# Kernel tuning notes

Measured on AMD Instinct MI355X. Metric: run time of the kernel, lower is better.

Reference implementation:

```python
import jax, jax.numpy as jnp
import numpy as np

B, S, H, NH, MLP = 4, 2048, 768, 12, 3072
HD = H // NH  # 64
EPS = 1e-6


def layernorm(x, w, b):
    m = jnp.mean(x, axis=-1, keepdims=True)
    v = jnp.mean(jnp.square(x - m), axis=-1, keepdims=True)
    return (x - m) * jax.lax.rsqrt(v + EPS) * w + b


def setup_inputs() -> dict:
    key = jax.random.key(0)
    ks = jax.random.split(key, 16)
    s = 0.02
    return {
        "x": jax.random.normal(ks[0], (B, S, H), dtype=jnp.float32),
        "ln1_w": jnp.ones((H,), jnp.float32),
        "ln1_b": jnp.zeros((H,), jnp.float32),
        "wq": jax.random.normal(ks[1], (H, H), jnp.float32) * s,
        "bq": jnp.zeros((H,), jnp.float32),
        "wk": jax.random.normal(ks[2], (H, H), jnp.float32) * s,
        "bk": jnp.zeros((H,), jnp.float32),
        "wv": jax.random.normal(ks[3], (H, H), jnp.float32) * s,
        "bv": jnp.zeros((H,), jnp.float32),
        "wo": jax.random.normal(ks[4], (H, H), jnp.float32) * s,
        "bo": jnp.zeros((H,), jnp.float32),
        "ln2_w": jnp.ones((H,), jnp.float32),
        "ln2_b": jnp.zeros((H,), jnp.float32),
        "w1": jax.random.normal(ks[5], (H, MLP), jnp.float32) * s,
        "b1": jnp.zeros((MLP,), jnp.float32),
        "w2": jax.random.normal(ks[6], (MLP, H), jnp.float32) * s,
        "b2": jnp.zeros((H,), jnp.float32),
    }


def reference(x, ln1_w, ln1_b, wq, bq, wk, bk, wv, bv, wo, bo,
              ln2_w, ln2_b, w1, b1, w2, b2):
    # --- attention sub-block (pre-norm) ---
    h = x
    xn = layernorm(x, ln1_w, ln1_b)
    q = (xn @ wq + bq).reshape(B, S, NH, HD)
    k = (xn @ wk + bk).reshape(B, S, NH, HD)
    v = (xn @ wv + bv).reshape(B, S, NH, HD)
    scores = jnp.einsum('bqhd,bkhd->bhqk', q, k) / jnp.sqrt(jnp.float32(HD))
    probs = jax.nn.softmax(scores, axis=-1)  # [B,NH,S,S] materialized, as in source
    ctx = jnp.einsum('bhqk,bkhd->bqhd', probs, v).reshape(B, S, H)
    x = ctx @ wo + bo + h
    # --- MLP sub-block (pre-norm) ---
    h = x
    xn = layernorm(x, ln2_w, ln2_b)
    y = jax.nn.gelu(xn @ w1 + b1, approximate=False)  # nn.GELU default = exact erf
    x = y @ w2 + b2 + h
    return x
```

## Files before the change

kernel.cpp:

```cpp
#include <hip/hip_runtime.h>
#include <hip/hip_bf16.h>

#define B_ 4
#define S_ 2048
#define H_ 768
#define NH_ 12
#define HD_ 64
#define MLP_ 3072
#define M_ (B_*S_)

typedef float f32x4 __attribute__((ext_vector_type(4)));
typedef short bf16x8 __attribute__((ext_vector_type(8)));

__device__ __forceinline__ short f2bf(float f) {
  union { float f; unsigned u; } x; x.f = f;
  unsigned r = (x.u + 0x7fffu + ((x.u >> 16) & 1u)) >> 16;
  return (short)(unsigned short)r;
}

__device__ __forceinline__ float exp2g(float x) {
  float r; asm("v_exp_f32 %0, %1" : "=v"(r) : "v"(x)); return r;
}
__device__ __forceinline__ float rcpg(float x) {
  float r; asm("v_rcp_f32 %0, %1" : "=v"(r) : "v"(x)); return r;
}
__device__ __forceinline__ unsigned cvtpk(float a, float b) {
  unsigned r; asm("v_cvt_pk_bf16_f32 %0, %1, %2" : "=v"(r) : "v"(a), "v"(b)); return r;
}

typedef __attribute__((address_space(1))) const void gvoid;
typedef __attribute__((address_space(3))) void lvoid;
__device__ __forceinline__ void async16(const void* g, void* l) {
  __builtin_amdgcn_global_load_lds((gvoid*)g, (lvoid*)l, 16, 0, 0);
}

__device__ __forceinline__ int xcd_swz(int h, int nwg) {
  const int q = nwg >> 3, r = nwg & 7;
  const int xc = h & 7, i = h >> 3;
  return (xc < r ? xc * (q + 1) : r * (q + 1) + (xc - r) * q) + i;
}

__global__ __launch_bounds__(256)
void tcast(const float* __restrict__ in, short* __restrict__ out, int K, int N) {
  __shared__ float tile[32][33];
  const int n0 = blockIdx.x * 32, k0 = blockIdx.y * 32;
  const int tx = threadIdx.x, ty = threadIdx.y;
#pragma unroll
  for (int i = 0; i < 4; ++i)
    tile[ty * 4 + i][tx] = in[(size_t)(k0 + ty * 4 + i) * N + n0 + tx];
  __syncthreads();
#pragma unroll
  for (int i = 0; i < 4; ++i)
    out[(size_t)(n0 + ty * 4 + i) * K + k0 + tx] = f2bf(tile[tx][ty * 4 + i]);
}

__global__ __launch_bounds__(256)
void tcast4(const float* __restrict__ i0, const float* __restrict__ i1,
            const float* __restrict__ i2, const float* __restrict__ i3,
            short* __restrict__ o0, short* __restrict__ o1,
            short* __restrict__ o2, short* __restrict__ o3) {
  __shared__ float tile[32][33];
  const int z = blockIdx.z;
  const float* in = (z == 0) ? i0 : (z == 1) ? i1 : (z == 2) ? i2 : i3;
  short* out = (z == 0) ? o0 : (z == 1) ? o1 : (z == 2) ? o2 : o3;
  const int n0 = blockIdx.x * 32, k0 = blockIdx.y * 32;
  const int tx = threadIdx.x, ty = threadIdx.y;
#pragma unroll
  for (int i = 0; i < 4; ++i)
    tile[ty * 4 + i][tx] = in[(size_t)(k0 + ty * 4 + i) * 768 + n0 + tx];
  __syncthreads();
#pragma unroll
  for (int i = 0; i < 4; ++i)
    out[(size_t)(n0 + ty * 4 + i) * 768 + k0 + tx] = f2bf(tile[tx][ty * 4 + i]);
}

__device__ __forceinline__ float block_sum256(float v) {
  __shared__ float red[4];
#pragma unroll
  for (int o = 32; o > 0; o >>= 1) v += __shfl_down(v, o);
  if ((threadIdx.x & 63) == 0) red[threadIdx.x >> 6] = v;
  __syncthreads();
  v = red[0] + red[1] + red[2] + red[3];
  __syncthreads();
  return v;
}

__global__ __launch_bounds__(256)
void ln_fwd(const float* __restrict__ xin, const float* __restrict__ g,
            const float* __restrict__ bt, short* __restrict__ o) {
  const int row = blockIdx.x, t = threadIdx.x;
  const float* xr = xin + (size_t)row * H_;
  const float v0 = xr[t], v1 = xr[t + 256], v2 = xr[t + 512];
  const float mean = block_sum256(v0 + v1 + v2) * (1.0f / H_);
  const float d0 = v0 - mean, d1 = v1 - mean, d2 = v2 - mean;
  const float var = block_sum256(d0 * d0 + d1 * d1 + d2 * d2) * (1.0f / H_);
  const float rstd = rsqrtf(var + 1e-6f);
  short* orow = o + (size_t)row * H_;
  orow[t]       = f2bf(d0 * rstd * g[t] + bt[t]);
  orow[t + 256] = f2bf(d1 * rstd * g[t + 256] + bt[t + 256]);
  orow[t + 512] = f2bf(d2 * rstd * g[t + 512] + bt[t + 512]);
}

#define QSCALE 0.18033688011112042f
template<int MODE>
__global__ __launch_bounds__(256)
void gemm_bt(const short* __restrict__ A, const short* __restrict__ Bw,
             int K, int N,
             const float* __restrict__ b0, const float* __restrict__ b1,
             const float* __restrict__ b2,
             const float* __restrict__ resid,
             float* __restrict__ outf, short* __restrict__ outh,
             short* __restrict__ oq, short* __restrict__ ok2, short* __restrict__ ov) {
  __shared__ short As[2][128 * 64];
  __shared__ short Bs[2][64 * 64];
  const int tid = threadIdx.x;
  const int wv = tid >> 6, lane = tid & 63;
  const int lo = lane & 15, hi = lane >> 4;
  const int wr = wv >> 1, wc = wv & 1;

  const int GX = gridDim.x;
  const int logical = xcd_swz(blockIdx.y * GX + blockIdx.x, GX * gridDim.y);
  const int bn = logical % GX, bm = logical / GX;

  const short* Ab = A + (size_t)bm * 128 * K;
  const short* Bb = Bw + (size_t)bn * 64 * K;
  const int srow = lane >> 3;
  const int scol = ((lane & 7) ^ srow) * 8;

  auto stage = [&](int buf, int kt) {
#pragma unroll
    for (int c = 0; c < 4; ++c) {
      const int rb = wv * 32 + c * 8;
      async16(Ab + (size_t)(rb + srow) * K + kt + scol, &As[buf][rb * 64]);
    }
#pragma unroll
    for (int c = 0; c < 2; ++c) {
      const int rb = wv * 16 + c * 8;
      async16(Bb + (size_t)(rb + srow) * K + kt + scol, &Bs[buf][rb * 64]);
    }
  };

  f32x4 acc[4][2] = {};
  stage(0, 0);
  const int nIt = K >> 6;
  for (int it = 0; it < nIt; ++it) {
    __syncthreads();
    if (it + 1 < nIt) stage((it + 1) & 1, (it + 1) << 6);
    const short* as = As[it & 1];
    const short* bs = Bs[it & 1];
#pragma unroll
    for (int ks = 0; ks < 2; ++ks) {
      const int rc = (((ks * 4 + hi) ^ (lo & 7)) * 8);
      bf16x8 af[4], bfr[2];
#pragma unroll
      for (int m = 0; m < 4; ++m)
        af[m] = *(const bf16x8*)&as[(wr * 64 + m * 16 + lo) * 64 + rc];
#pragma unroll
      for (int n = 0; n < 2; ++n)
        bfr[n] = *(const bf16x8*)&bs[(wc * 32 + n * 16 + lo) * 64 + rc];
#pragma unroll
      for (int m = 0; m < 4; ++m)
#pragma unroll
        for (int n = 0; n < 2; ++n)
          acc[m][n] = __builtin_amdgcn_mfma_f32_16x16x32_bf16(af[m], bfr[n], acc[m][n], 0, 0, 0);
    }
  }
  const int colBase = bn * 64 + wc * 32;
  const int rowBase = bm * 128 + wr * 64;
#pragma unroll
  for (int m = 0; m < 4; ++m) {
#pragma unroll
    for (int n = 0; n < 2; ++n) {
#pragma unroll
      for (int r = 0; r < 4; ++r) {
        const int row = rowBase + m * 16 + hi * 4 + r;
        const int col = colBase + n * 16 + lo;
        float val = acc[m][n][r];
        if (MODE == 0) {
          const int which = col / H_;
          const int nn = col - which * H_;
          val += (which == 0 ? b0 : which == 1 ? b1 : b2)[nn];
          if (which == 0) val *= QSCALE;
          const int h = nn >> 6, d = nn & 63;
          const int bI = row >> 11, s = row & (S_ - 1);
          const short bv16 = f2bf(val);
          if (which == 2) {
            const int sl = s & 63;
            const int pc = ((sl >> 4) & 1) * 32 + ((sl >> 2) & 3) * 8
                         + ((sl >> 5) & 1) * 4 + (sl & 3);
            ov[(((size_t)bI * NH_ + h) * HD_ + d) * S_ + (s & ~63) + pc] = bv16;
          } else {
            short* dst = (which == 0 ? oq : ok2);
            dst[(((size_t)bI * NH_ + h) * S_ + s) * HD_ + d] = bv16;
          }
        } else if (MODE == 1) {
          val += b0[col] + resid[(size_t)row * N + col];
          outf[(size_t)row * N + col] = val;
        } else {
          val += b0[col];
          const float u = val * (0.7978845608f + 0.0356774081f * val * val);
          const float e = exp2g(-2.885390082f * u);
          val = val * rcpg(1.0f + e);
          outh[(size_t)row * N + col] = f2bf(val);
        }
      }
    }
  }
}

__global__ __launch_bounds__(256)
void attn_fwd(const short* __restrict__ qbuf, const short* __restrict__ kbuf,
              const short* __restrict__ vbuf, short* __restrict__ ctx) {
  __shared__ short Ks[2][8 * 512];
  __shared__ short Vt[2][8 * 512];
  const int tid = threadIdx.x;
  const int wv = tid >> 6, lane = tid & 63;
  const int lo = lane & 15, hi = lane >> 4;
  const int logical = xcd_swz(blockIdx.y * 32 + blockIdx.x, 32 * 48);
  const int qt = logical & 31, bh = logical >> 5;
  const int bI = bh / NH_, h = bh - bI * NH_;
  const size_t baseBH = (size_t)bh * S_ * HD_;
  const int q0 = qt * 64 + wv * 16;

  bf16x8 qf[2];
#pragma unroll
  for (int ks = 0; ks < 2; ++ks)
    qf[ks] = *(const bf16x8*)&qbuf[baseBH + (size_t)(q0 + lo) * HD_ + ks * 32 + hi * 8];

  f32x4 accc[4] = {};
  f32x4 accS = {};
  float mrow = 0.0f;

  const short oo = (lo == 0) ? (short)0x3F80 : (short)0;
  const bf16x8 onesf = {oo, oo, oo, oo, oo, oo, oo, oo};

  const short* ksrc = kbuf + baseBH + (size_t)(wv * 16 + lo) * HD_ + hi * 8;
  const short* vsrc = vbuf + baseBH + (size_t)(wv * 16 + lo) * S_ + hi * 8;
  const int dst0 = wv * 1024 + lane * 8;

  bf16x8 kreg0, kreg1, vreg0, vreg1;
  kreg0 = *(const bf16x8*)(ksrc);
  kreg1 = *(const bf16x8*)(ksrc + 32);
  vreg0 = *(const bf16x8*)(vsrc);
  vreg1 = *(const bf16x8*)(vsrc + 32);
  *(bf16x8*)&Ks[0][dst0] = kreg0;
  *(bf16x8*)&Ks[0][dst0 + 512] = kreg1;
  *(bf16x8*)&Vt[0][dst0] = vreg0;
  *(bf16x8*)&Vt[0][dst0 + 512] = vreg1;
  kreg0 = *(const bf16x8*)(ksrc + (size_t)64 * HD_);
  kreg1 = *(const bf16x8*)(ksrc + (size_t)64 * HD_ + 32);
  vreg0 = *(const bf16x8*)(vsrc + 64);
  vreg1 = *(const bf16x8*)(vsrc + 64 + 32);
  __syncthreads();

  for (int t = 0; t < S_ / 64; ++t) {
    const int cur = t & 1, nxt = cur ^ 1;
    const short* ks = Ks[cur];
    const short* vt = Vt[cur];
    f32x4 sc[4];
    __builtin_amdgcn_s_setprio(1);
#pragma unroll
    for (int nk = 0; nk < 4; ++nk) {
      f32x4 z = {0.f, 0.f, 0.f, 0.f};
#pragma unroll
      for (int k2 = 0; k2 < 2; ++k2) {
        bf16x8 kf = *(const bf16x8*)&ks[(nk * 2 + k2) * 512 + lane * 8];
        z = __builtin_amdgcn_mfma_f32_16x16x32_bf16(kf, qf[k2], z, 0, 0, 0);
      }
      sc[nk] = z;
    }
    __builtin_amdgcn_s_setprio(0);
    *(bf16x8*)&Ks[nxt][dst0] = kreg0;
    *(bf16x8*)&Ks[nxt][dst0 + 512] = kreg1;
    *(bf16x8*)&Vt[nxt][dst0] = vreg0;
    *(bf16x8*)&Vt[nxt][dst0 + 512] = vreg1;
    {
      const int tn = (t + 2 < S_ / 64) ? t + 2 : S_ / 64 - 1;
      const short* kp = ksrc + (size_t)tn * 64 * HD_;
      kreg0 = *(const bf16x8*)(kp);
      kreg1 = *(const bf16x8*)(kp + 32);
      const short* vp = vsrc + tn * 64;
      vreg0 = *(const bf16x8*)(vp);
      vreg1 = *(const bf16x8*)(vp + 32);
    }
    const float m0 = fmaxf(fmaxf(sc[0][0], sc[0][1]), fmaxf(sc[0][2], sc[0][3]));
    const float m1 = fmaxf(fmaxf(sc[1][0], sc[1][1]), fmaxf(sc[1][2], sc[1][3]));
    const float m2 = fmaxf(fmaxf(sc[2][0], sc[2][1]), fmaxf(sc[2][2], sc[2][3]));
    const float m3 = fmaxf(fmaxf(sc[3][0], sc[3][1]), fmaxf(sc[3][2], sc[3][3]));
    float mx = fmaxf(fmaxf(m0, m1), fmaxf(m2, m3));
#pragma unroll
    for (int nk = 0; nk < 4; ++nk)
#pragma unroll
      for (int r = 0; r < 4; ++r)
        sc[nk][r] = exp2g(sc[nk][r] - mrow);
    if (!__all(mx <= mrow + 8.0f)) {
      mx = fmaxf(mx, __shfl_xor(mx, 16));
      mx = fmaxf(mx, __shfl_xor(mx, 32));
      const float mnew = fmaxf(mrow, mx);
      const float alpha = exp2g(mrow - mnew);
#pragma unroll
      for (int nk = 0; nk < 4; ++nk)
#pragma unroll
        for (int r = 0; r < 4; ++r) sc[nk][r] *= alpha;
#pragma unroll
      for (int r = 0; r < 4; ++r) {
        const float aA = __shfl(alpha, hi * 4 + r);
        accS[r] *= aA;
#pragma unroll
        for (int nd = 0; nd < 4; ++nd) accc[nd][r] *= aA;
      }
      mrow = mnew;
    }
    union PU { unsigned u[4]; bf16x8 v; } pa0, pa1;
    pa0.u[0] = cvtpk(sc[0][0], sc[0][1]); pa0.u[1] = cvtpk(sc[0][2], sc[0][3]);
    pa0.u[2] = cvtpk(sc[2][0], sc[2][1]); pa0.u[3] = cvtpk(sc[2][2], sc[2][3]);
    pa1.u[0] = cvtpk(sc[1][0], sc[1][1]); pa1.u[1] = cvtpk(sc[1][2], sc[1][3]);
    pa1.u[2] = cvtpk(sc[3][0], sc[3][1]); pa1.u[3] = cvtpk(sc[3][2], sc[3][3]);
    __builtin_amdgcn_s_setprio(1);
    accS = __builtin_amdgcn_mfma_f32_16x16x32_bf16(pa0.v, onesf, accS, 0, 0, 0);
    accS = __builtin_amdgcn_mfma_f32_16x16x32_bf16(pa1.v, onesf, accS, 0, 0, 0);
#pragma unroll
    for (int nd = 0; nd < 4; ++nd) {
      bf16x8 vf0 = *(const bf16x8*)&vt[(nd * 2 + 0) * 512 + lane * 8];
      accc[nd] = __builtin_amdgcn_mfma_f32_16x16x32_bf16(pa0.v, vf0, accc[nd], 0, 0, 0);
      bf16x8 vf1 = *(const bf16x8*)&vt[(nd * 2 + 1) * 512 + lane * 8];
      accc[nd] = __builtin_amdgcn_mfma_f32_16x16x32_bf16(pa1.v, vf1, accc[nd], 0, 0, 0);
    }
    __builtin_amdgcn_s_setprio(0);
    __syncthreads();
  }
#pragma unroll
  for (int r = 0; r < 4; ++r) {
    const float inv = 1.0f / __shfl(accS[r], hi << 4);
    const int srow = q0 + hi * 4 + r;
    const size_t rowoff = ((size_t)bI * S_ + srow) * H_ + h * HD_;
#pragma unroll
    for (int nd = 0; nd < 4; ++nd)
      ctx[rowoff + nd * 16 + lo] = f2bf(accc[nd][r] * inv);
  }
}

extern "C" void kernel_launch(void* const* d_in, const int* in_sizes, int n_in,
                              void* d_out, int out_size, void* d_ws, size_t ws_size,
                              hipStream_t stream) {
  const float* x    = (const float*)d_in[0];
  const float* ln1w = (const float*)d_in[1];
  const float* ln1b = (const float*)d_in[2];
  const float* wq   = (const float*)d_in[3];
  const float* bq   = (const float*)d_in[4];
  const float* wk   = (const float*)d_in[5];
  const float* bk   = (const float*)d_in[6];
  const float* wvp  = (const float*)d_in[7];
  const float* bv   = (const float*)d_in[8];
  const float* wo   = (const float*)d_in[9];
  const float* bo   = (const float*)d_in[10];
  const float* ln2w = (const float*)d_in[11];
  const float* ln2b = (const float*)d_in[12];
  const float* w1   = (const float*)d_in[13];
  const float* b1   = (const float*)d_in[14];
  const float* w2   = (const float*)d_in[15];
  const float* b2   = (const float*)d_in[16];
  float* out = (float*)d_out;

  short* ws = (short*)d_ws;
  short* wqkvT = ws;
  short* woT   = wqkvT + (size_t)2304 * 768;
  short* w1T   = woT + (size_t)768 * 768;
  short* w2T   = w1T + (size_t)3072 * 768;
  short* xn    = w2T + (size_t)768 * 3072;
  short* qb    = xn + (size_t)M_ * H_;
  short* kb    = qb + (size_t)M_ * H_;
  short* vb    = kb + (size_t)M_ * H_;
  short* ctx   = vb + (size_t)M_ * H_;
  short* yb    = qb;
  float* x1    = (float*)(ctx + (size_t)M_ * H_);

  dim3 tb(32, 8);
  tcast4<<<dim3(24, 24, 4), tb, 0, stream>>>(wq, wk, wvp, wo,
      wqkvT, wqkvT + (size_t)768 * 768, wqkvT + (size_t)2 * 768 * 768, woT);
  tcast<<<dim3(96, 24), tb, 0, stream>>>(w1, w1T, 768, 3072);
  tcast<<<dim3(24, 96), tb, 0, stream>>>(w2, w2T, 3072, 768);

  ln_fwd<<<M_, 256, 0, stream>>>(x, ln1w, ln1b, xn);

  gemm_bt<0><<<dim3(36, 64), 256, 0, stream>>>(xn, wqkvT, 768, 2304,
      bq, bk, bv, nullptr, nullptr, nullptr, qb, kb, vb);

  attn_fwd<<<dim3(32, 48), 256, 0, stream>>>(qb, kb, vb, ctx);

  gemm_bt<1><<<dim3(12, 64), 256, 0, stream>>>(ctx, woT, 768, 768,
      bo, nullptr, nullptr, x, x1, nullptr, nullptr, nullptr, nullptr);

  ln_fwd<<<M_, 256, 0, stream>>>(x1, ln2w, ln2b, xn);

  gemm_bt<2><<<dim3(48, 64), 256, 0, stream>>>(xn, w1T, 768, 3072,
      b1, nullptr, nullptr, nullptr, nullptr, yb, nullptr, nullptr, nullptr);

  gemm_bt<1><<<dim3(12, 64), 256, 0, stream>>>(yb, w2T, 3072, 768,
      b2, nullptr, nullptr, x1, out, nullptr, nullptr, nullptr, nullptr);
}
```

Baseline: 316.9 us.

## Process two query tiles per attention block and fold running max into MFMA init

Each attention workgroup now handles 128 query rows (two 16-row sets per wave) instead of 64, so every K/V tile loaded into shared memory feeds twice as many MFMAs and the grid halves. The negative running max is preloaded into the score accumulator, which removes the subtraction before exp2, and rescaling now works per lane with no alpha shuffles. The row max uses v_max3 and the final normalisation uses v_rcp. In exchange it uses more registers, which may lower occupancy, and the smaller grid gives fewer waves to spread across CUs.

```diff
diff --git a/kernel.cpp b/kernel.cpp
--- a/kernel.cpp
+++ b/kernel.cpp
@@ -23,6 +23,9 @@
 }
 __device__ __forceinline__ float rcpg(float x) {
   float r; asm("v_rcp_f32 %0, %1" : "=v"(r) : "v"(x)); return r;
+}
+__device__ __forceinline__ float max3g(float a, float b, float c) {
+  float r; asm("v_max3_f32 %0, %1, %2, %3" : "=v"(r) : "v"(a), "v"(b), "v"(c)); return r;
 }
 __device__ __forceinline__ unsigned cvtpk(float a, float b) {
   unsigned r; asm("v_cvt_pk_bf16_f32 %0, %1, %2" : "=v"(r) : "v"(a), "v"(b)); return r;
@@ -216,20 +219,22 @@
   const int tid = threadIdx.x;
   const int wv = tid >> 6, lane = tid & 63;
   const int lo = lane & 15, hi = lane >> 4;
-  const int logical = xcd_swz(blockIdx.y * 32 + blockIdx.x, 32 * 48);
-  const int qt = logical & 31, bh = logical >> 5;
+  const int logical = xcd_swz(blockIdx.y * 16 + blockIdx.x, 16 * 48);
+  const int qt = logical & 15, bh = logical >> 4;
   const int bI = bh / NH_, h = bh - bI * NH_;
   const size_t baseBH = (size_t)bh * S_ * HD_;
-  const int q0 = qt * 64 + wv * 16;
-
-  bf16x8 qf[2];
-#pragma unroll
-  for (int ks = 0; ks < 2; ++ks)
-    qf[ks] = *(const bf16x8*)&qbuf[baseBH + (size_t)(q0 + lo) * HD_ + ks * 32 + hi * 8];
-
-  f32x4 accc[4] = {};
-  f32x4 accS = {};
-  float mrow = 0.0f;
+  const int q0 = qt * 128 + wv * 16;
+
+  bf16x8 qfA[2], qfB[2];
+#pragma unroll
+  for (int k2 = 0; k2 < 2; ++k2) {
+    qfA[k2] = *(const bf16x8*)&qbuf[baseBH + (size_t)(q0 + lo) * HD_ + k2 * 32 + hi * 8];
+    qfB[k2] = *(const bf16x8*)&qbuf[baseBH + (size_t)(q0 + 64 + lo) * HD_ + k2 * 32 + hi * 8];
+  }
+
+  f32x4 accA[4] = {}, accB[4] = {};
+  f32x4 accSA = {}, accSB = {};
+  float nmA = 0.0f, nmB = 0.0f;
 
   const short oo = (lo == 0) ? (short)0x3F80 : (short)0;
   const bf16x8 onesf = {oo, oo, oo, oo, oo, oo, oo, oo};
@@ -257,17 +262,20 @@
     const int cur = t & 1, nxt = cur ^ 1;
     const short* ks = Ks[cur];
     const short* vt = Vt[cur];
-    f32x4 sc[4];
+    const f32x4 ciA = {nmA, nmA, nmA, nmA};
+    const f32x4 ciB = {nmB, nmB, nmB, nmB};
+    f32x4 scA[4], scB[4];
     __builtin_amdgcn_s_setprio(1);
 #pragma unroll
     for (int nk = 0; nk < 4; ++nk) {
-      f32x4 z = {0.f, 0.f, 0.f, 0.f};
+      f32x4 zA = ciA, zB = ciB;
 #pragma unroll
       for (int k2 = 0; k2 < 2; ++k2) {
         bf16x8 kf = *(const bf16x8*)&ks[(nk * 2 + k2) * 512 + lane * 8];
-        z = __builtin_amdgcn_mfma_f32_16x16x32_bf16(kf, qf[k2], z, 0, 0, 0);
+        zA = __builtin_amdgcn_mfma_f32_16x16x32_bf16(kf, qfA[k2], zA, 0, 0, 0);
+        zB = __builtin_amdgcn_mfma_f32_16x16x32_bf16(kf, qfB[k2], zB, 0, 0, 0);
       }
-      sc[nk] = z;
+      scA[nk] = zA; scB[nk] = zB;
     }
     __builtin_amdgcn_s_setprio(0);
     *(bf16x8*)&Ks[nxt][dst0] = kreg0;
@@ -283,60 +291,83 @@
       vreg0 = *(const bf16x8*)(vp);
       vreg1 = *(const bf16x8*)(vp + 32);
     }
-    const float m0 = fmaxf(fmaxf(sc[0][0], sc[0][1]), fmaxf(sc[0][2], sc[0][3]));
-    const float m1 = fmaxf(fmaxf(sc[1][0], sc[1][1]), fmaxf(sc[1][2], sc[1][3]));
-    const float m2 = fmaxf(fmaxf(sc[2][0], sc[2][1]), fmaxf(sc[2][2], sc[2][3]));
-    const float m3 = fmaxf(fmaxf(sc[3][0], sc[3][1]), fmaxf(sc[3][2], sc[3][3]));
-    float mx = fmaxf(fmaxf(m0, m1), fmaxf(m2, m3));
+    float mxA = max3g(scA[0][0], scA[0][1], scA[0][2]);
+    mxA = max3g(mxA, scA[0][3], scA[1][0]);
+    mxA = max3g(mxA, scA[1][1], scA[1][2]);
+    mxA = max3g(mxA, scA[1][3], scA[2][0]);
+    mxA = max3g(mxA, scA[2][1], scA[2][2]);
+    mxA = max3g(mxA, scA[2][3], scA[3][0]);
+    mxA = max3g(mxA, scA[3][1], scA[3][2]);
+    mxA = fmaxf(mxA, scA[3][3]);
+    float mxB = max3g(scB[0][0], scB[0][1], scB[0][2]);
+    mxB = max3g(mxB, scB[0][3], scB[1][0]);
+    mxB = max3g(mxB, scB[1][1], scB[1][2]);
+    mxB = max3g(mxB, scB[1][3], scB[2][0]);
+    mxB = max3g(mxB, scB[2][1], scB[2][2]);
+    mxB = max3g(mxB, scB[2][3], scB[3][0]);
+    mxB = max3g(mxB, scB[3][1], scB[3][2]);
+    mxB = fmaxf(mxB, scB[3][3]);
 #pragma unroll
     for (int nk = 0; nk < 4; ++nk)
 #pragma unroll
-      for (int r = 0; r < 4; ++r)
-        sc[nk][r] = exp2g(sc[nk][r] - mrow);
-    if (!__all(mx <= mrow + 8.0f)) {
-      mx = fmaxf(mx, __shfl_xor(mx, 16));
-      mx = fmaxf(mx, __shfl_xor(mx, 32));
-      const float mnew = fmaxf(mrow, mx);
-      const float alpha = exp2g(mrow - mnew);
+      for (int r = 0; r < 4; ++r) {
+        scA[nk][r] = exp2g(scA[nk][r]);
+        scB[nk][r] = exp2g(scB[nk][r]);
+      }
+    if (!__all(fmaxf(mxA, mxB) <= 8.0f)) {
+      mxA = fmaxf(mxA, __shfl_xor(mxA, 16));
+      mxA = fmaxf(mxA, __shfl_xor(mxA, 32));
+      mxB = fmaxf(mxB, __shfl_xor(mxB, 16));
+      mxB = fmaxf(mxB, __shfl_xor(mxB, 32));
+      const float dA = fmaxf(mxA, 0.0f), dB = fmaxf(mxB, 0.0f);
+      const float aA = exp2g(-dA), aB = exp2g(-dB);
+      nmA -= dA; nmB -= dB;
 #pragma unroll
       for (int nk = 0; nk < 4; ++nk)
 #pragma unroll
-        for (int r = 0; r < 4; ++r) sc[nk][r] *= alpha;
-#pragma unroll
-      for (int r = 0; r < 4; ++r) {
-        const float aA = __shfl(alpha, hi * 4 + r);
-        accS[r] *= aA;
-#pragma unroll
-        for (int nd = 0; nd < 4; ++nd) accc[nd][r] *= aA;
-      }
-      mrow = mnew;
-    }
-    union PU { unsigned u[4]; bf16x8 v; } pa0, pa1;
-    pa0.u[0] = cvtpk(sc[0][0], sc[0][1]); pa0.u[1] = cvtpk(sc[0][2], sc[0][3]);
-    pa0.u[2] = cvtpk(sc[2][0], sc[2][1]); pa0.u[3] = cvtpk(sc[2][2], sc[2][3]);
-    pa1.u[0] = cvtpk(sc[1][0], sc[1][1]); pa1.u[1] = cvtpk(sc[1][2], sc[1][3]);
-    pa1.u[2] = cvtpk(sc[3][0], sc[3][1]); pa1.u[3] = cvtpk(sc[3][2], sc[3][3]);
+        for (int r = 0; r < 4; ++r) { scA[nk][r] *= aA; scB[nk][r] *= aB; }
+      accSA *= aA; accSB *= aB;
+#pragma unroll
+      for (int nd = 0; nd < 4; ++nd) { accA[nd] *= aA; accB[nd] *= aB; }
+    }
+    union PU { unsigned u[4]; bf16x8 v; } pA0, pA1, pB0, pB1;
+    pA0.u[0] = cvtpk(scA[0][0], scA[0][1]); pA0.u[1] = cvtpk(scA[0][2], scA[0][3]);
+    pA0.u[2] = cvtpk(scA[2][0], scA[2][1]); pA0.u[3] = cvtpk(scA[2][2], scA[2][3]);
+    pA1.u[0] = cvtpk(scA[1][0], scA[1][1]); pA1.u[1] = cvtpk(scA[1][2], scA[1][3]);
+    pA1.u[2] = cvtpk(scA[3][0], scA[3][1]); pA1.u[3] = cvtpk(scA[3][2], scA[3][3]);
+    pB0.u[0] = cvtpk(scB[0][0], scB[0][1]); pB0.u[1] = cvtpk(scB[0][2], scB[0][3]);
+    pB0.u[2] = cvtpk(scB[2][0], scB[2][1]); pB0.u[3] = cvtpk(scB[2][2], scB[2][3]);
+    pB1.u[0] = cvtpk(scB[1][0], scB[1][1]); pB1.u[1] = cvtpk(scB[1][2], scB[1][3]);
+    pB1.u[2] = cvtpk(scB[3][0], scB[3][1]); pB1.u[3] = cvtpk(scB[3][2], scB[3][3]);
     __builtin_amdgcn_s_setprio(1);
-    accS = __builtin_amdgcn_mfma_f32_16x16x32_bf16(pa0.v, onesf, accS, 0, 0, 0);
-    accS = __builtin_amdgcn_mfma_f32_16x16x32_bf16(pa1.v, onesf, accS, 0, 0, 0);
+    accSA = __builtin_amdgcn_mfma_f32_16x16x32_bf16(pA0.v, onesf, accSA, 0, 0, 0);
+    accSA = __builtin_amdgcn_mfma_f32_16x16x32_bf16(pA1.v, onesf, accSA, 0, 0, 0);
+    accSB = __builtin_amdgcn_mfma_f32_16x16x32_bf16(pB0.v, onesf, accSB, 0, 0, 0);
+    accSB = __builtin_amdgcn_mfma_f32_16x16x32_bf16(pB1.v, onesf, accSB, 0, 0, 0);
 #pragma unroll
     for (int nd = 0; nd < 4; ++nd) {
       bf16x8 vf0 = *(const bf16x8*)&vt[(nd * 2 + 0) * 512 + lane * 8];
-      accc[nd] = __builtin_amdgcn_mfma_f32_16x16x32_bf16(pa0.v, vf0, accc[nd], 0, 0, 0);
+      accA[nd] = __builtin_amdgcn_mfma_f32_16x16x32_bf16(pA0.v, vf0, accA[nd], 0, 0, 0);
+      accB[nd] = __builtin_amdgcn_mfma_f32_16x16x32_bf16(pB0.v, vf0, accB[nd], 0, 0, 0);
       bf16x8 vf1 = *(const bf16x8*)&vt[(nd * 2 + 1) * 512 + lane * 8];
-      accc[nd] = __builtin_amdgcn_mfma_f32_16x16x32_bf16(pa1.v, vf1, accc[nd], 0, 0, 0);
+      accA[nd] = __builtin_amdgcn_mfma_f32_16x16x32_bf16(pA1.v, vf1, accA[nd], 0, 0, 0);
+      accB[nd] = __builtin_amdgcn_mfma_f32_16x16x32_bf16(pB1.v, vf1, accB[nd], 0, 0, 0);
     }
     __builtin_amdgcn_s_setprio(0);
     __syncthreads();
   }
 #pragma unroll
   for (int r = 0; r < 4; ++r) {
-    const float inv = 1.0f / __shfl(accS[r], hi << 4);
-    const int srow = q0 + hi * 4 + r;
-    const size_t rowoff = ((size_t)bI * S_ + srow) * H_ + h * HD_;
-#pragma unroll
-    for (int nd = 0; nd < 4; ++nd)
-      ctx[rowoff + nd * 16 + lo] = f2bf(accc[nd][r] * inv);
+    const float invA = rcpg(__shfl(accSA[r], hi << 4));
+    const float invB = rcpg(__shfl(accSB[r], hi << 4));
+    const int srA = q0 + hi * 4 + r;
+    const size_t roA = ((size_t)bI * S_ + srA) * H_ + h * HD_;
+    const size_t roB = ((size_t)bI * S_ + srA + 64) * H_ + h * HD_;
+#pragma unroll
+    for (int nd = 0; nd < 4; ++nd) {
+      ctx[roA + nd * 16 + lo] = f2bf(accA[nd][r] * invA);
+      ctx[roB + nd * 16 + lo] = f2bf(accB[nd][r] * invB);
+    }
   }
 }
 
@@ -386,7 +417,7 @@
   gemm_bt<0><<<dim3(36, 64), 256, 0, stream>>>(xn, wqkvT, 768, 2304,
       bq, bk, bv, nullptr, nullptr, nullptr, qb, kb, vb);
 
-  attn_fwd<<<dim3(32, 48), 256, 0, stream>>>(qb, kb, vb, ctx);
+  attn_fwd<<<dim3(16, 48), 256, 0, stream>>>(qb, kb, vb, ctx);
 
   gemm_bt<1><<<dim3(12, 64), 256, 0, stream>>>(ctx, woT, 768, 768,
       bo, nullptr, nullptr, x, x1, nullptr, nullptr, nullptr, nullptr);
```

Result: faster. 288.1 us (-9.1%).
